# Kernel tuning notes

Hardware: AMD Instinct MI355X
Metric: run time of the kernel (lower is better)

The kernel has to match this reference:

```python
import jax, jax.numpy as jnp
import numpy as np

N_NODES = 100000
N_EDGES = 1600000
IN_CH = 128
HID = 128


def setup_inputs() -> dict:
    key = jax.random.key(0)
    ks = jax.random.split(key, 8)
    x = jax.random.normal(ks[0], (N_NODES, IN_CH), dtype=jnp.float32)
    edge_index = jax.random.randint(ks[1], (2, N_EDGES), 0, N_NODES, dtype=jnp.int64)
    # GCNConv weights (glorot-ish scale) and biases; readout Linear(HID, 1)
    s1 = 1.0 / np.sqrt(IN_CH)
    s2 = 1.0 / np.sqrt(HID)
    W1 = jax.random.normal(ks[2], (IN_CH, HID), dtype=jnp.float32) * s1
    b1 = jnp.zeros((HID,), dtype=jnp.float32)
    W2 = jax.random.normal(ks[3], (HID, HID), dtype=jnp.float32) * s2
    b2 = jnp.zeros((HID,), dtype=jnp.float32)
    Wout = jax.random.normal(ks[4], (HID, 1), dtype=jnp.float32) * s2
    bout = jnp.zeros((1,), dtype=jnp.float32)
    return {"x": x, "edge_index": edge_index, "W1": W1, "b1": b1,
            "W2": W2, "b2": b2, "Wout": Wout, "bout": bout}


def _gcn_conv(x, W, b, src, dst, norm, n_nodes):
    # x' = D^{-1/2}(A+I)D^{-1/2} (x W) + b   (PyG GCNConv default)
    h = x @ W                                   # [N, out]
    msg = h[src] * norm[:, None]                # gather + edge-wise scale
    agg = jax.ops.segment_sum(msg, dst, num_segments=n_nodes)  # scatter-add
    return agg + b


def reference(x, edge_index, W1, b1, W2, b2, Wout, bout):
    n = x.shape[0]
    loop = jnp.arange(n, dtype=edge_index.dtype)
    src = jnp.concatenate([edge_index[0], loop])  # source nodes j (+ self-loops)
    dst = jnp.concatenate([edge_index[1], loop])  # target nodes i (+ self-loops)
    deg = jax.ops.segment_sum(jnp.ones_like(dst, dtype=x.dtype), dst, num_segments=n)
    dis = jax.lax.rsqrt(deg)  # deg >= 1 due to self-loops
    norm = dis[src] * dis[dst]
    h = jax.nn.relu(_gcn_conv(x, W1, b1, src, dst, norm, n))
    h = jax.nn.relu(_gcn_conv(h, W2, b2, src, dst, norm, n))
    out = h @ Wout + bout                        # [N, 1]
    return jnp.squeeze(out)                      # [N]
```

## Files before the change

kernel.cpp:

```cpp
#include <hip/hip_runtime.h>
#include <hip/hip_fp16.h>
#include <type_traits>

#define NFEAT 128
#define SRC_BITS 17
#define SRC_MASK ((1u << SRC_BITS) - 1u)
#define BUKSH 8
#define CHUNK 8192
#define STHREADS 512
#define KG 32

using f16x8 = __attribute__((ext_vector_type(8))) _Float16;
using f32x4 = __attribute__((ext_vector_type(4))) float;

static inline size_t align_up(size_t x, size_t a) { return (x + a - 1) & ~(a - 1); }


__global__ __launch_bounds__(STHREADS) void k_hist(const int* __restrict__ dst,
                                                   int* __restrict__ gh,
                                                   int NBUK, int E) {
  extern __shared__ int h[];
  for (int i = threadIdx.x; i < NBUK; i += STHREADS) h[i] = 0;
  __syncthreads();
  int base = blockIdx.x * CHUNK;
  int end = min(base + CHUNK, E);
  for (int e = base + threadIdx.x; e < end; e += STHREADS)
    atomicAdd(&h[dst[e] >> BUKSH], 1);
  __syncthreads();
  int* out = gh + (size_t)blockIdx.x * NBUK;
  for (int i = threadIdx.x; i < NBUK; i += STHREADS) out[i] = h[i];
}

__global__ __launch_bounds__(256) void k_colscan_part(int* __restrict__ gh,
                                                      int* __restrict__ psum,
                                                      int NBUK, int nblk) {
  int b = blockIdx.y * 256 + threadIdx.x;
  if (b >= NBUK) return;
  int kg = blockIdx.x;
  int k0 = kg * KG, k1 = min(k0 + KG, nblk);
  int run = 0;
  for (int k = k0; k < k1; ++k) {
    int idx = k * NBUK + b;
    int c = gh[idx];
    gh[idx] = run;
    run += c;
  }
  psum[kg * NBUK + b] = run;
}

__global__ __launch_bounds__(512) void k_colscan_fix2(int* __restrict__ psum,
                                                      int* __restrict__ rsB,
                                                      int NBUK, int NG, int E) {
  __shared__ int sd[512];
  int b = threadIdx.x;
  int tot = 0;
  if (b < NBUK) {
    int run = 0;
    for (int kg = 0; kg < NG; ++kg) {
      int idx = kg * NBUK + b;
      int c = psum[idx];
      psum[idx] = run;
      run += c;
    }
    tot = run;
  }
  sd[b] = tot;
  __syncthreads();
  for (int off = 1; off < 512; off <<= 1) {
    int t = (b >= off) ? sd[b - off] : 0;
    __syncthreads();
    sd[b] += t;
    __syncthreads();
  }
  if (b < NBUK) rsB[b] = sd[b] - tot;
  if (b == 0) rsB[NBUK] = E;
}

__global__ __launch_bounds__(STHREADS) void k_scatter(const int* __restrict__ src,
                                                      const int* __restrict__ dst,
                                                      const int* __restrict__ gh,
                                                      const int* __restrict__ psum,
                                                      const int* __restrict__ rsB,
                                                      unsigned* __restrict__ ebuf,
                                                      int NBUK, int E) {
  extern __shared__ int cur[];
  const int* g = gh + (size_t)blockIdx.x * NBUK;
  const int* p = psum + (size_t)(blockIdx.x / KG) * NBUK;
  for (int i = threadIdx.x; i < NBUK; i += STHREADS) cur[i] = rsB[i] + p[i] + g[i];
  __syncthreads();
  int base = blockIdx.x * CHUNK;
  int end = min(base + CHUNK, E);
  for (int e = base + threadIdx.x; e < end; e += STHREADS) {
    int d = dst[e];
    int pos = atomicAdd(&cur[d >> BUKSH], 1);
    ebuf[pos] = (unsigned)src[e] | ((unsigned)(d & 255) << SRC_BITS);
  }
}

__global__ __launch_bounds__(256) void k_fill3(const unsigned* __restrict__ ebuf,
                                               const int* __restrict__ rsB,
                                               int* __restrict__ rs,
                                               float* __restrict__ dis,
                                               int* __restrict__ csrc, int N) {
  __shared__ int hist[256];
  __shared__ int curs[256];
  __shared__ int sd[256];
  int b = blockIdx.x;
  int node0 = b << BUKSH;
  int nn = min(256, N - node0);
  int base = rsB[b], end = rsB[b + 1];
  int tid = threadIdx.x;
  hist[tid] = 0;
  __syncthreads();
  for (int e = base + tid; e < end; e += 256)
    atomicAdd(&hist[ebuf[e] >> SRC_BITS], 1);
  __syncthreads();
  int c = hist[tid];
  sd[tid] = c;
  __syncthreads();
  for (int off = 1; off < 256; off <<= 1) {
    int t = (tid >= off) ? sd[tid - off] : 0;
    __syncthreads();
    sd[tid] += t;
    __syncthreads();
  }
  int start = base + sd[tid] - c;
  curs[tid] = start;
  hist[tid] = start;
  __syncthreads();
  if (tid < nn) {
    int nxt = (tid == nn - 1) ? end : hist[tid + 1];
    rs[node0 + tid] = start;
    dis[node0 + tid] = rsqrtf((float)(nxt - start) + 1.0f);
  }
  if (tid == 0) rs[node0 + nn] = end;
  for (int e = base + tid; e < end; e += 256) {
    unsigned u = ebuf[e];
    int pos = atomicAdd(&curs[u >> SRC_BITS], 1);
    csrc[pos] = (int)(u & SRC_MASK);
  }
}


__global__ __launch_bounds__(256) void k_wt2(const float* __restrict__ W1,
                                             const float* __restrict__ W2,
                                             __half* __restrict__ W1t,
                                             __half* __restrict__ W2t) {
  int m = blockIdx.x >> 4;
  const float* W = m ? W2 : W1;
  __half* Wt = m ? W2t : W1t;
  int o = (blockIdx.x & 15) * 1024 + threadIdx.x * 4;
  #pragma unroll
  for (int j = 0; j < 4; ++j) {
    int oo = o + j;
    int cdst = oo >> 7, rdst = oo & 127;
    Wt[oo] = __float2half(W[rdst * 128 + cdst]);
  }
}


#define XS_LD 136

template <typename T>
__global__ __launch_bounds__(256) void k_gemm(const T* __restrict__ X,
                                              const __half* __restrict__ Wt,
                                              const float* __restrict__ dis,
                                              __half* __restrict__ P, int N) {
  __shared__ __half Xs[64 * XS_LD];
  __shared__ __half Ws[128 * XS_LD];
  const int tid = threadIdx.x;
  const int wave = tid >> 6, lane = tid & 63;
  const int l15 = lane & 15, g = lane >> 4;
  const int rowBase = blockIdx.x * 64;

  #pragma unroll
  for (int it = 0; it < 8; ++it) {
    int q = it * 256 + tid;
    int r = q >> 4, c = (q & 15) * 8;
    *(int4*)&Ws[r * XS_LD + c] = *(const int4*)(Wt + r * 128 + c);
  }
  if constexpr (std::is_same_v<T, float>) {
    #pragma unroll
    for (int it = 0; it < 8; ++it) {
      int q = it * 256 + tid;
      int r = q >> 5, c = (q & 31) * 4;
      int gr = rowBase + r;
      float4 v = make_float4(0.f, 0.f, 0.f, 0.f);
      if (gr < N) v = *(const float4*)(X + (size_t)gr * NFEAT + c);
      __half2 pk[2];
      pk[0] = __floats2half2_rn(v.x, v.y);
      pk[1] = __floats2half2_rn(v.z, v.w);
      *(uint2*)&Xs[r * XS_LD + c] = *(uint2*)pk;
    }
  } else {
    #pragma unroll
    for (int it = 0; it < 4; ++it) {
      int q = it * 256 + tid;
      int r = q >> 4, c = (q & 15) * 8;
      int gr = rowBase + r;
      int4 v = make_int4(0, 0, 0, 0);
      if (gr < N) v = *(const int4*)(X + (size_t)gr * NFEAT + c);
      *(int4*)&Xs[r * XS_LD + c] = v;
    }
  }
  __syncthreads();

  f32x4 acc[4][2];
  #pragma unroll
  for (int rt = 0; rt < 4; ++rt) {
    acc[rt][0] = (f32x4)(0.f);
    acc[rt][1] = (f32x4)(0.f);
  }
  const int koff = g * 8;
  const int c0 = (wave * 2) * 16 + l15;
  const int c1 = (wave * 2 + 1) * 16 + l15;

  #pragma unroll
  for (int ks = 0; ks < 4; ++ks) {
    int kb = ks * 32 + koff;
    f16x8 b0 = *(const f16x8*)&Ws[c0 * XS_LD + kb];
    f16x8 b1 = *(const f16x8*)&Ws[c1 * XS_LD + kb];
    #pragma unroll
    for (int rt = 0; rt < 4; ++rt) {
      f16x8 a = *(const f16x8*)&Xs[(rt * 16 + l15) * XS_LD + kb];
      acc[rt][0] = __builtin_amdgcn_mfma_f32_16x16x32_f16(a, b0, acc[rt][0], 0, 0, 0);
      acc[rt][1] = __builtin_amdgcn_mfma_f32_16x16x32_f16(a, b1, acc[rt][1], 0, 0, 0);
    }
  }

  const int colb = wave * 32 + l15;
  #pragma unroll
  for (int rt = 0; rt < 4; ++rt) {
    #pragma unroll
    for (int r = 0; r < 4; ++r) {
      int row = rowBase + rt * 16 + g * 4 + r;
      if (row < N) {
        float di = dis[row];
        P[(size_t)row * NFEAT + colb]      = __float2half(di * acc[rt][0][r]);
        P[(size_t)row * NFEAT + colb + 16] = __float2half(di * acc[rt][1][r]);
      }
    }
  }
}


__device__ __forceinline__ float agg_body_h4(const __half* __restrict__ P,
                                             const int* __restrict__ rs,
                                             const int* __restrict__ csrc,
                                             int w, int g, int li, float facc[8]) {
  int e0 = rs[w], e1 = rs[w + 1];
  float di = rsqrtf((float)(e1 - e0) + 1.0f);
  __half2 a0 = __float2half2_rn(0.f), a1 = a0, a2 = a0, a3 = a0;
  __half2 c0 = a0, c1 = a0, c2 = a0, c3 = a0;
  if (g == 0) {
    int4 raw = *(const int4*)(P + (size_t)w * NFEAT + li * 8);
    const __half2* h2 = (const __half2*)&raw;
    a0 = h2[0]; a1 = h2[1]; a2 = h2[2]; a3 = h2[3];
  }
  const int lastc = max(e1 - 1, 0);
  int e = e0 + g;
  int s0 = csrc[min(e, lastc)];
  int s1 = csrc[min(e + 4, lastc)];
  int s2 = csrc[min(e + 8, lastc)];
  int s3 = csrc[min(e + 12, lastc)];
  while (e + 12 < e1) {
    int4 r0 = *(const int4*)(P + (size_t)s0 * NFEAT + li * 8);
    int4 r1 = *(const int4*)(P + (size_t)s1 * NFEAT + li * 8);
    int4 r2 = *(const int4*)(P + (size_t)s2 * NFEAT + li * 8);
    int4 r3 = *(const int4*)(P + (size_t)s3 * NFEAT + li * 8);
    e += 16;
    s0 = csrc[min(e, lastc)];
    s1 = csrc[min(e + 4, lastc)];
    s2 = csrc[min(e + 8, lastc)];
    s3 = csrc[min(e + 12, lastc)];
    const __half2* h0 = (const __half2*)&r0;
    const __half2* h1 = (const __half2*)&r1;
    const __half2* h2 = (const __half2*)&r2;
    const __half2* h3 = (const __half2*)&r3;
    a0 = __hadd2(a0, h0[0]); a1 = __hadd2(a1, h0[1]);
    a2 = __hadd2(a2, h0[2]); a3 = __hadd2(a3, h0[3]);
    c0 = __hadd2(c0, h1[0]); c1 = __hadd2(c1, h1[1]);
    c2 = __hadd2(c2, h1[2]); c3 = __hadd2(c3, h1[3]);
    a0 = __hadd2(a0, h2[0]); a1 = __hadd2(a1, h2[1]);
    a2 = __hadd2(a2, h2[2]); a3 = __hadd2(a3, h2[3]);
    c0 = __hadd2(c0, h3[0]); c1 = __hadd2(c1, h3[1]);
    c2 = __hadd2(c2, h3[2]); c3 = __hadd2(c3, h3[3]);
  }
  if (e < e1) {
    int4 r = *(const int4*)(P + (size_t)s0 * NFEAT + li * 8);
    const __half2* h = (const __half2*)&r;
    a0 = __hadd2(a0, h[0]); a1 = __hadd2(a1, h[1]);
    a2 = __hadd2(a2, h[2]); a3 = __hadd2(a3, h[3]);
    e += 4;
  }
  if (e < e1) {
    int4 r = *(const int4*)(P + (size_t)s1 * NFEAT + li * 8);
    const __half2* h = (const __half2*)&r;
    c0 = __hadd2(c0, h[0]); c1 = __hadd2(c1, h[1]);
    c2 = __hadd2(c2, h[2]); c3 = __hadd2(c3, h[3]);
    e += 4;
  }
  if (e < e1) {
    int4 r = *(const int4*)(P + (size_t)s2 * NFEAT + li * 8);
    const __half2* h = (const __half2*)&r;
    a0 = __hadd2(a0, h[0]); a1 = __hadd2(a1, h[1]);
    a2 = __hadd2(a2, h[2]); a3 = __hadd2(a3, h[3]);
  }
  a0 = __hadd2(a0, c0); a1 = __hadd2(a1, c1);
  a2 = __hadd2(a2, c2); a3 = __hadd2(a3, c3);
  float2 f0 = __half22float2(a0), f1 = __half22float2(a1);
  float2 f2 = __half22float2(a2), f3 = __half22float2(a3);
  facc[0] = f0.x; facc[1] = f0.y; facc[2] = f1.x; facc[3] = f1.y;
  facc[4] = f2.x; facc[5] = f2.y; facc[6] = f3.x; facc[7] = f3.y;
  #pragma unroll
  for (int j = 0; j < 8; ++j) {
    float v = facc[j];
    v += __shfl_xor(v, 16, 64);
    v += __shfl_xor(v, 32, 64);
    facc[j] = v;
  }
  return di;
}

__global__ __launch_bounds__(256) void k_agg_relu(const __half* __restrict__ P,
                                                  const int* __restrict__ rs,
                                                  const int* __restrict__ csrc,
                                                  const float* __restrict__ bias,
                                                  __half* __restrict__ Hout, int N) {
  int w = (blockIdx.x * 256 + threadIdx.x) >> 6;
  if (w >= N) return;
  int lane = threadIdx.x & 63;
  int g = lane >> 4, li = lane & 15;
  float acc[8];
  float di = agg_body_h4(P, rs, csrc, w, g, li, acc);
  if (g == 0) {
    float4 b0 = *(const float4*)(bias + li * 8);
    float4 b1 = *(const float4*)(bias + li * 8 + 4);
    __half2 o[4];
    o[0] = __floats2half2_rn(fmaxf(fmaf(di, acc[0], b0.x), 0.f),
                             fmaxf(fmaf(di, acc[1], b0.y), 0.f));
    o[1] = __floats2half2_rn(fmaxf(fmaf(di, acc[2], b0.z), 0.f),
                             fmaxf(fmaf(di, acc[3], b0.w), 0.f));
    o[2] = __floats2half2_rn(fmaxf(fmaf(di, acc[4], b1.x), 0.f),
                             fmaxf(fmaf(di, acc[5], b1.y), 0.f));
    o[3] = __floats2half2_rn(fmaxf(fmaf(di, acc[6], b1.z), 0.f),
                             fmaxf(fmaf(di, acc[7], b1.w), 0.f));
    *(int4*)(Hout + (size_t)w * NFEAT + li * 8) = *(const int4*)o;
  }
}

__global__ __launch_bounds__(256) void k_agg_readout(const __half* __restrict__ P,
                                                     const int* __restrict__ rs,
                                                     const int* __restrict__ csrc,
                                                     const float* __restrict__ bias,
                                                     const float* __restrict__ Wout,
                                                     const float* __restrict__ bout,
                                                     float* __restrict__ out, int N) {
  int w = (blockIdx.x * 256 + threadIdx.x) >> 6;
  if (w >= N) return;
  int lane = threadIdx.x & 63;
  int g = lane >> 4, li = lane & 15;
  float acc[8];
  float di = agg_body_h4(P, rs, csrc, w, g, li, acc);
  float4 b0 = *(const float4*)(bias + li * 8);
  float4 b1 = *(const float4*)(bias + li * 8 + 4);
  float4 w0 = *(const float4*)(Wout + li * 8);
  float4 w1 = *(const float4*)(Wout + li * 8 + 4);
  float p = 0.f;
  p = fmaf(fmaxf(fmaf(di, acc[0], b0.x), 0.f), w0.x, p);
  p = fmaf(fmaxf(fmaf(di, acc[1], b0.y), 0.f), w0.y, p);
  p = fmaf(fmaxf(fmaf(di, acc[2], b0.z), 0.f), w0.z, p);
  p = fmaf(fmaxf(fmaf(di, acc[3], b0.w), 0.f), w0.w, p);
  p = fmaf(fmaxf(fmaf(di, acc[4], b1.x), 0.f), w1.x, p);
  p = fmaf(fmaxf(fmaf(di, acc[5], b1.y), 0.f), w1.y, p);
  p = fmaf(fmaxf(fmaf(di, acc[6], b1.z), 0.f), w1.z, p);
  p = fmaf(fmaxf(fmaf(di, acc[7], b1.w), 0.f), w1.w, p);
  p += __shfl_down(p, 8, 64);
  p += __shfl_down(p, 4, 64);
  p += __shfl_down(p, 2, 64);
  p += __shfl_down(p, 1, 64);
  if (lane == 0) out[w] = p + bout[0];
}


extern "C" void kernel_launch(void* const* d_in, const int* in_sizes, int n_in,
                              void* d_out, int out_size, void* d_ws, size_t ws_size,
                              hipStream_t stream) {
  const float* x    = (const float*)d_in[0];
  const int*   ei   = (const int*)d_in[1];
  const float* W1   = (const float*)d_in[2];
  const float* b1   = (const float*)d_in[3];
  const float* W2   = (const float*)d_in[4];
  const float* b2   = (const float*)d_in[5];
  const float* Wout = (const float*)d_in[6];
  const float* bout = (const float*)d_in[7];
  float* out = (float*)d_out;

  const int N = in_sizes[0] / NFEAT;
  const int E = in_sizes[1] / 2;
  const int* src = ei;
  const int* dst = ei + E;
  const int NBUK = (N + 255) >> BUKSH;
  const int nblk = (E + CHUNK - 1) / CHUNK;
  const int NG = (nblk + KG - 1) / KG;

  char* ws = (char*)d_ws;
  size_t off = 0;
  auto alloc = [&](size_t bytes) -> char* {
    char* p = ws + off;
    off = align_up(off + bytes, 256);
    return p;
  };
  int*      gh    = (int*)alloc((size_t)nblk * NBUK * 4);
  int*      psum  = (int*)alloc((size_t)NG * NBUK * 4);
  int*      rsB   = (int*)alloc((size_t)(NBUK + 1) * 4);
  int*      rs    = (int*)alloc((size_t)(N + 1) * 4);
  float*    dis   = (float*)alloc((size_t)N * 4);
  unsigned* ebuf  = (unsigned*)alloc((size_t)E * 4);
  int*      csrc  = (int*)alloc((size_t)E * 4);
  __half*   W1t   = (__half*)alloc((size_t)NFEAT * NFEAT * 2);
  __half*   W2t   = (__half*)alloc((size_t)NFEAT * NFEAT * 2);
  __half*   P1    = (__half*)alloc((size_t)N * NFEAT * 2);
  __half*   H     = (__half*)alloc((size_t)N * NFEAT * 2);
  (void)ws_size; (void)n_in; (void)out_size;

  const size_t ldsBuk = (size_t)NBUK * 4;
  const int bukBlks = (NBUK + 255) / 256;

  k_wt2<<<32, 256, 0, stream>>>(W1, W2, W1t, W2t);
  k_hist<<<nblk, STHREADS, ldsBuk, stream>>>(dst, gh, NBUK, E);
  k_colscan_part<<<dim3(NG, bukBlks), 256, 0, stream>>>(gh, psum, NBUK, nblk);
  k_colscan_fix2<<<1, 512, 0, stream>>>(psum, rsB, NBUK, NG, E);
  k_scatter<<<nblk, STHREADS, ldsBuk, stream>>>(src, dst, gh, psum, rsB, ebuf, NBUK, E);
  k_fill3<<<NBUK, 256, 0, stream>>>(ebuf, rsB, rs, dis, csrc, N);

  k_gemm<float><<<(N + 63) / 64, 256, 0, stream>>>(x, W1t, dis, P1, N);
  k_agg_relu<<<(N + 3) / 4, 256, 0, stream>>>(P1, rs, csrc, b1, H, N);
  k_gemm<__half><<<(N + 63) / 64, 256, 0, stream>>>(H, W2t, dis, P1, N);
  k_agg_readout<<<(N + 3) / 4, 256, 0, stream>>>(P1, rs, csrc, b2, Wout, bout, out, N);
}
```

Measured before the change: 218.8 us.

## Fuse graph preprocessing kernels into one cooperative kernel with grid syncs

```diff
diff --git a/kernel.cpp b/kernel.cpp
--- a/kernel.cpp
+++ b/kernel.cpp
@@ -1,13 +1,15 @@
 #include <hip/hip_runtime.h>
 #include <hip/hip_fp16.h>
+#include <hip/hip_cooperative_groups.h>
 #include <type_traits>
+
+namespace cg = cooperative_groups;
 
 #define NFEAT 128
 #define SRC_BITS 17
 #define SRC_MASK ((1u << SRC_BITS) - 1u)
 #define BUKSH 8
 #define CHUNK 8192
-#define STHREADS 512
 #define KG 32
 
 using f16x8 = __attribute__((ext_vector_type(8))) _Float16;
@@ -16,145 +18,151 @@
 static inline size_t align_up(size_t x, size_t a) { return (x + a - 1) & ~(a - 1); }
 
 
-__global__ __launch_bounds__(STHREADS) void k_hist(const int* __restrict__ dst,
-                                                   int* __restrict__ gh,
-                                                   int NBUK, int E) {
-  extern __shared__ int h[];
-  for (int i = threadIdx.x; i < NBUK; i += STHREADS) h[i] = 0;
-  __syncthreads();
-  int base = blockIdx.x * CHUNK;
-  int end = min(base + CHUNK, E);
-  for (int e = base + threadIdx.x; e < end; e += STHREADS)
-    atomicAdd(&h[dst[e] >> BUKSH], 1);
-  __syncthreads();
-  int* out = gh + (size_t)blockIdx.x * NBUK;
-  for (int i = threadIdx.x; i < NBUK; i += STHREADS) out[i] = h[i];
-}
-
-__global__ __launch_bounds__(256) void k_colscan_part(int* __restrict__ gh,
-                                                      int* __restrict__ psum,
-                                                      int NBUK, int nblk) {
-  int b = blockIdx.y * 256 + threadIdx.x;
-  if (b >= NBUK) return;
-  int kg = blockIdx.x;
-  int k0 = kg * KG, k1 = min(k0 + KG, nblk);
-  int run = 0;
-  for (int k = k0; k < k1; ++k) {
-    int idx = k * NBUK + b;
-    int c = gh[idx];
-    gh[idx] = run;
-    run += c;
-  }
-  psum[kg * NBUK + b] = run;
-}
-
-__global__ __launch_bounds__(512) void k_colscan_fix2(int* __restrict__ psum,
-                                                      int* __restrict__ rsB,
-                                                      int NBUK, int NG, int E) {
-  __shared__ int sd[512];
-  int b = threadIdx.x;
-  int tot = 0;
-  if (b < NBUK) {
-    int run = 0;
-    for (int kg = 0; kg < NG; ++kg) {
-      int idx = kg * NBUK + b;
-      int c = psum[idx];
-      psum[idx] = run;
-      run += c;
-    }
-    tot = run;
-  }
-  sd[b] = tot;
-  __syncthreads();
-  for (int off = 1; off < 512; off <<= 1) {
-    int t = (b >= off) ? sd[b - off] : 0;
-    __syncthreads();
-    sd[b] += t;
-    __syncthreads();
-  }
-  if (b < NBUK) rsB[b] = sd[b] - tot;
-  if (b == 0) rsB[NBUK] = E;
-}
-
-__global__ __launch_bounds__(STHREADS) void k_scatter(const int* __restrict__ src,
-                                                      const int* __restrict__ dst,
-                                                      const int* __restrict__ gh,
-                                                      const int* __restrict__ psum,
-                                                      const int* __restrict__ rsB,
-                                                      unsigned* __restrict__ ebuf,
-                                                      int NBUK, int E) {
-  extern __shared__ int cur[];
-  const int* g = gh + (size_t)blockIdx.x * NBUK;
-  const int* p = psum + (size_t)(blockIdx.x / KG) * NBUK;
-  for (int i = threadIdx.x; i < NBUK; i += STHREADS) cur[i] = rsB[i] + p[i] + g[i];
-  __syncthreads();
-  int base = blockIdx.x * CHUNK;
-  int end = min(base + CHUNK, E);
-  for (int e = base + threadIdx.x; e < end; e += STHREADS) {
-    int d = dst[e];
-    int pos = atomicAdd(&cur[d >> BUKSH], 1);
-    ebuf[pos] = (unsigned)src[e] | ((unsigned)(d & 255) << SRC_BITS);
-  }
-}
-
-__global__ __launch_bounds__(256) void k_fill3(const unsigned* __restrict__ ebuf,
-                                               const int* __restrict__ rsB,
-                                               int* __restrict__ rs,
-                                               float* __restrict__ dis,
-                                               int* __restrict__ csrc, int N) {
-  __shared__ int hist[256];
-  __shared__ int curs[256];
-  __shared__ int sd[256];
-  int b = blockIdx.x;
-  int node0 = b << BUKSH;
-  int nn = min(256, N - node0);
-  int base = rsB[b], end = rsB[b + 1];
-  int tid = threadIdx.x;
-  hist[tid] = 0;
-  __syncthreads();
-  for (int e = base + tid; e < end; e += 256)
-    atomicAdd(&hist[ebuf[e] >> SRC_BITS], 1);
-  __syncthreads();
-  int c = hist[tid];
-  sd[tid] = c;
-  __syncthreads();
-  for (int off = 1; off < 256; off <<= 1) {
-    int t = (tid >= off) ? sd[tid - off] : 0;
-    __syncthreads();
-    sd[tid] += t;
-    __syncthreads();
-  }
-  int start = base + sd[tid] - c;
-  curs[tid] = start;
-  hist[tid] = start;
-  __syncthreads();
-  if (tid < nn) {
-    int nxt = (tid == nn - 1) ? end : hist[tid + 1];
-    rs[node0 + tid] = start;
-    dis[node0 + tid] = rsqrtf((float)(nxt - start) + 1.0f);
-  }
-  if (tid == 0) rs[node0 + nn] = end;
-  for (int e = base + tid; e < end; e += 256) {
-    unsigned u = ebuf[e];
-    int pos = atomicAdd(&curs[u >> SRC_BITS], 1);
-    csrc[pos] = (int)(u & SRC_MASK);
-  }
-}
-
-
-__global__ __launch_bounds__(256) void k_wt2(const float* __restrict__ W1,
-                                             const float* __restrict__ W2,
-                                             __half* __restrict__ W1t,
-                                             __half* __restrict__ W2t) {
-  int m = blockIdx.x >> 4;
-  const float* W = m ? W2 : W1;
-  __half* Wt = m ? W2t : W1t;
-  int o = (blockIdx.x & 15) * 1024 + threadIdx.x * 4;
-  #pragma unroll
-  for (int j = 0; j < 4; ++j) {
-    int oo = o + j;
-    int cdst = oo >> 7, rdst = oo & 127;
-    Wt[oo] = __float2half(W[rdst * 128 + cdst]);
+__global__ __launch_bounds__(512) void k_prep(const float* __restrict__ W1,
+                                              const float* __restrict__ W2,
+                                              __half* __restrict__ W1t,
+                                              __half* __restrict__ W2t,
+                                              const int* __restrict__ src,
+                                              const int* __restrict__ dst,
+                                              int* __restrict__ gh,
+                                              int* __restrict__ psum,
+                                              int* __restrict__ rsB,
+                                              int* __restrict__ rs,
+                                              float* __restrict__ dis,
+                                              unsigned* __restrict__ ebuf,
+                                              int* __restrict__ csrc,
+                                              int NBUK, int nblk, int NG, int N, int E) {
+  cg::grid_group grid = cg::this_grid();
+  extern __shared__ int lds[];
+  const int tid = threadIdx.x;
+  const int bid = blockIdx.x;
+  const int nb = gridDim.x;
+
+  {
+    int g = bid * 512 + tid;
+    if (g < 32768) {
+      int m = g >> 14;
+      int oo = g & 16383;
+      const float* W = m ? W2 : W1;
+      __half* Wt = m ? W2t : W1t;
+      int cdst = oo >> 7, rdst = oo & 127;
+      Wt[oo] = __float2half(W[rdst * 128 + cdst]);
+    }
+  }
+  {
+    for (int i = tid; i < NBUK; i += 512) lds[i] = 0;
+    __syncthreads();
+    int base = bid * CHUNK;
+    int end = min(base + CHUNK, E);
+    for (int e = base + tid; e < end; e += 512)
+      atomicAdd(&lds[dst[e] >> BUKSH], 1);
+    __syncthreads();
+    int* outp = gh + (size_t)bid * NBUK;
+    for (int i = tid; i < NBUK; i += 512) outp[i] = lds[i];
+  }
+  grid.sync();
+
+  {
+    int t = bid * 512 + tid;
+    if (t < NG * NBUK) {
+      int kg = t / NBUK;
+      int b = t - kg * NBUK;
+      int k0 = kg * KG, k1 = min(k0 + KG, nblk);
+      int run = 0;
+      for (int k = k0; k < k1; ++k) {
+        int idx = k * NBUK + b;
+        int c = gh[idx];
+        gh[idx] = run;
+        run += c;
+      }
+      psum[kg * NBUK + b] = run;
+    }
+  }
+  grid.sync();
+
+  if (bid == 0) {
+    __shared__ int sd[512];
+    int b = tid;
+    int tot = 0;
+    if (b < NBUK) {
+      int run = 0;
+      for (int kg = 0; kg < NG; ++kg) {
+        int idx = kg * NBUK + b;
+        int c = psum[idx];
+        psum[idx] = run;
+        run += c;
+      }
+      tot = run;
+    }
+    sd[b] = tot;
+    __syncthreads();
+    for (int off = 1; off < 512; off <<= 1) {
+      int t2 = (b >= off) ? sd[b - off] : 0;
+      __syncthreads();
+      sd[b] += t2;
+      __syncthreads();
+    }
+    if (b < NBUK) rsB[b] = sd[b] - tot;
+    if (b == 0) rsB[NBUK] = E;
+  }
+  grid.sync();
+
+  {
+    const int* g = gh + (size_t)bid * NBUK;
+    const int* p = psum + (size_t)(bid / KG) * NBUK;
+    for (int i = tid; i < NBUK; i += 512) lds[i] = rsB[i] + p[i] + g[i];
+    __syncthreads();
+    int base = bid * CHUNK;
+    int end = min(base + CHUNK, E);
+    for (int e = base + tid; e < end; e += 512) {
+      int d = dst[e];
+      int pos = atomicAdd(&lds[d >> BUKSH], 1);
+      ebuf[pos] = (unsigned)src[e] | ((unsigned)(d & 255) << SRC_BITS);
+    }
+  }
+  grid.sync();
+
+  for (int b = bid; b < NBUK; b += nb) {
+    int* hist = lds;
+    int* curs = lds + 256;
+    int* sd2  = lds + 512;
+    int node0 = b << BUKSH;
+    int nn = min(256, N - node0);
+    int base = rsB[b], end = rsB[b + 1];
+    __syncthreads();
+    if (tid < 256) hist[tid] = 0;
+    __syncthreads();
+    for (int e = base + tid; e < end; e += 512)
+      atomicAdd(&hist[ebuf[e] >> SRC_BITS], 1);
+    __syncthreads();
+    if (tid < 256) sd2[tid] = hist[tid];
+    __syncthreads();
+    for (int off = 1; off < 256; off <<= 1) {
+      int t2 = 0;
+      if (tid < 256 && tid >= off) t2 = sd2[tid - off];
+      __syncthreads();
+      if (tid < 256) sd2[tid] += t2;
+      __syncthreads();
+    }
+    if (tid < 256) {
+      int c = hist[tid];
+      int start = base + sd2[tid] - c;
+      curs[tid] = start;
+      hist[tid] = start;
+    }
+    __syncthreads();
+    if (tid < nn) {
+      int start = hist[tid];
+      int nxt = (tid == nn - 1) ? end : hist[tid + 1];
+      rs[node0 + tid] = start;
+      dis[node0 + tid] = rsqrtf((float)(nxt - start) + 1.0f);
+    }
+    if (tid == 0) rs[node0 + nn] = end;
+    for (int e = base + tid; e < end; e += 512) {
+      unsigned u = ebuf[e];
+      int pos = atomicAdd(&curs[u >> SRC_BITS], 1);
+      csrc[pos] = (int)(u & SRC_MASK);
+    }
   }
 }
 
@@ -424,15 +432,18 @@
   __half*   H     = (__half*)alloc((size_t)N * NFEAT * 2);
   (void)ws_size; (void)n_in; (void)out_size;
 
-  const size_t ldsBuk = (size_t)NBUK * 4;
-  const int bukBlks = (NBUK + 255) / 256;
-
-  k_wt2<<<32, 256, 0, stream>>>(W1, W2, W1t, W2t);
-  k_hist<<<nblk, STHREADS, ldsBuk, stream>>>(dst, gh, NBUK, E);
-  k_colscan_part<<<dim3(NG, bukBlks), 256, 0, stream>>>(gh, psum, NBUK, nblk);
-  k_colscan_fix2<<<1, 512, 0, stream>>>(psum, rsB, NBUK, NG, E);
-  k_scatter<<<nblk, STHREADS, ldsBuk, stream>>>(src, dst, gh, psum, rsB, ebuf, NBUK, E);
-  k_fill3<<<NBUK, 256, 0, stream>>>(ebuf, rsB, rs, dis, csrc, N);
+  {
+    int nbuk = NBUK, nbk = nblk, ng = NG, n = N, e = E;
+    void* args[] = {
+      (void*)&W1, (void*)&W2, (void*)&W1t, (void*)&W2t,
+      (void*)&src, (void*)&dst,
+      (void*)&gh, (void*)&psum, (void*)&rsB, (void*)&rs, (void*)&dis,
+      (void*)&ebuf, (void*)&csrc,
+      (void*)&nbuk, (void*)&nbk, (void*)&ng, (void*)&n, (void*)&e,
+    };
+    hipLaunchCooperativeKernel((const void*)k_prep, dim3(nblk), dim3(512),
+                               args, 768 * sizeof(int), stream);
+  }
 
   k_gemm<float><<<(N + 63) / 64, 256, 0, stream>>>(x, W1t, dis, P1, N);
   k_agg_relu<<<(N + 3) / 4, 256, 0, stream>>>(P1, rs, csrc, b1, H, N);
```

Result: slower. 313.7 us (+43.4%).
